# Kernel optimization log

Hardware: AMD Instinct MI355X
Metric: run time of the kernel (lower is better)

Reference implementation:

```python
import jax, jax.numpy as jnp
import numpy as np

ALPHA = 0.2          # LeakyReLU negative slope (Alpha)
NEG_INF = -9e15      # mask value used by pygat-style GAT


def _masked_attention(Wh, a_src, a_dst, mask):
    """Wh: [H,N,d], a_src/a_dst: [H,d], mask: [N,N] (nonzero = edge).
    Returns attention-aggregated features [H,N,d]."""
    f_src = jnp.einsum('hnd,hd->hn', Wh, a_src)   # [H,N]
    f_dst = jnp.einsum('hnd,hd->hn', Wh, a_dst)   # [H,N]
    e = jax.nn.leaky_relu(f_src[:, :, None] + f_dst[:, None, :], ALPHA)  # [H,N,N]
    e = jnp.where(mask[None, :, :] > 0, e, NEG_INF)
    att = jax.nn.softmax(e, axis=-1)              # masked softmax over neighbors
    return jnp.einsum('hnm,hmd->hnd', att, Wh)    # [H,N,d]


def setup_inputs() -> dict:
    key = jax.random.key(0)
    ks = jax.random.split(key, 8)
    N, F_in, D, H = 4096, 512, 64, 8
    x = jax.random.normal(ks[0], (N, F_in), dtype=jnp.float32)
    adj = jax.random.randint(ks[1], (N, N), 0, 2, dtype=jnp.int32)
    s = 0.1
    W = jax.random.normal(ks[2], (H, F_in, D), dtype=jnp.float32) * s
    a_src = jax.random.normal(ks[3], (H, D), dtype=jnp.float32) * s
    a_dst = jax.random.normal(ks[4], (H, D), dtype=jnp.float32) * s
    W_o = jax.random.normal(ks[5], (H * D, D), dtype=jnp.float32) * s
    ao_src = jax.random.normal(ks[6], (D,), dtype=jnp.float32) * s
    ao_dst = jax.random.normal(ks[7], (D,), dtype=jnp.float32) * s
    return {"x": x, "adj": adj, "W": W, "a_src": a_src, "a_dst": a_dst,
            "W_o": W_o, "ao_src": ao_src, "ao_dst": ao_dst}


def reference(x, adj, W, a_src, a_dst, W_o, ao_src, ao_dst):
    N = x.shape[0]
    # --- multi-head layer (concat=True: ELU per head, concat on feature dim) ---
    Wh = jnp.einsum('nf,hfd->hnd', x, W)                     # [H,N,d]
    h1 = jax.nn.elu(_masked_attention(Wh, a_src, a_dst, adj))  # [H,N,d]
    h_cat = jnp.transpose(h1, (1, 0, 2)).reshape(N, -1)      # [N, H*d]
    # --- output head (concat=False: no ELU inside layer) ---
    Who = (h_cat @ W_o)[None]                                # [1,N,d]
    h2 = _masked_attention(Who, ao_src[None], ao_dst[None], adj)[0]  # [N,d]
    # GAT.forward: activation (ELU) then log_softmax over dim=1
    return jax.nn.log_softmax(jax.nn.elu(h2), axis=1)
```

## Files before the change

### kernel.cpp

```cpp
#include <hip/hip_runtime.h>
#include <hip/hip_bf16.h>
#include <math.h>

#define N_NODES 4096
#define FDIM 512
#define D 64
#define H 8
#define NWORDS (N_NODES / 64)

typedef __attribute__((ext_vector_type(8))) short bf16x8;
typedef __attribute__((ext_vector_type(4))) float f32x4;

__device__ inline short f2bf(float x) {
    return (short)((__builtin_bit_cast(unsigned int, x) + 0x8000u) >> 16);
}
__device__ inline float b2f(unsigned short s) {
    return __builtin_bit_cast(float, (unsigned int)s << 16);
}

__device__ inline int sext_bit(unsigned int v, int j) {
#if defined(__has_builtin) && __has_builtin(__builtin_amdgcn_sbfe)
    return __builtin_amdgcn_sbfe((int)v, j, 1);
#else
    return ((int)(v << (31 - j))) >> 31;
#endif
}

__device__ inline unsigned fenc(float f) {
    unsigned u = __builtin_bit_cast(unsigned, f);
    return (u & 0x80000000u) ? ~u : (u | 0x80000000u);
}
__device__ inline float fdec(unsigned e) {
    unsigned u = (e & 0x80000000u) ? (e & 0x7FFFFFFFu) : ~e;
    return __builtin_bit_cast(float, u);
}

__device__ inline void gl2lds16(const void* g, void* l) {
#if defined(__has_builtin) && __has_builtin(__builtin_amdgcn_global_load_lds)
    __builtin_amdgcn_global_load_lds(
        (const __attribute__((address_space(1))) unsigned int*)g,
        (__attribute__((address_space(3))) unsigned int*)l, 16, 0, 0);
#else
    *(uint4*)l = *(const uint4*)g;
#endif
}

#define NB_BITS (N_NODES * N_NODES / 2048)
#define NB_X    (N_NODES * FDIM / 1024)
#define NB_W    (H * FDIM * D / 256)
#define NB_WO   (FDIM * D / 256)
__global__ void k_pre(const int* __restrict__ adj, const float* __restrict__ x,
                      const float* __restrict__ W, const float* __restrict__ Wo,
                      unsigned int* __restrict__ bits32, short* __restrict__ Xbf,
                      short* __restrict__ WF, short* __restrict__ WoF,
                      float* __restrict__ cm1, float* __restrict__ cm2,
                      unsigned* __restrict__ gmaxe1, unsigned* __restrict__ gmaxe2) {
    const int b = blockIdx.x, t = threadIdx.x;
    if (b == 0) {
        for (int i = t; i < H * D; i += 256) cm1[i] = 0.f;
        if (t < D) cm2[t] = 0.f;
        if (t < H) gmaxe1[t] = 0u;
        if (t == 0) gmaxe2[0] = 0u;
        return;
    }
    if (b < 1 + NB_BITS) {
        const int tid  = (b - 1) * 256 + t;
        const size_t e0 = (size_t)tid * 8;
        int4 a0 = *(const int4*)&adj[e0];
        int4 a1 = *(const int4*)&adj[e0 + 4];
        unsigned by = (unsigned)(a0.x != 0)       | ((unsigned)(a0.y != 0) << 1)
                    | ((unsigned)(a0.z != 0) << 2) | ((unsigned)(a0.w != 0) << 3)
                    | ((unsigned)(a1.x != 0) << 4) | ((unsigned)(a1.y != 0) << 5)
                    | ((unsigned)(a1.z != 0) << 6) | ((unsigned)(a1.w != 0) << 7);
        unsigned v = by | (__shfl_xor((int)by, 1) << 8);
        v = v | ((unsigned)__shfl_xor((int)v, 2) << 16);
        if ((t & 3) == 0) bits32[tid >> 2] = v;
        return;
    }
    if (b < 1 + NB_BITS + NB_X) {
        const size_t i4 = ((size_t)(b - 1 - NB_BITS) * 256 + t) * 4;
        float4 v = *(const float4*)&x[i4];
        ushort4 o;
        o.x = (unsigned short)f2bf(v.x); o.y = (unsigned short)f2bf(v.y);
        o.z = (unsigned short)f2bf(v.z); o.w = (unsigned short)f2bf(v.w);
        *(ushort4*)&Xbf[i4] = o;
        return;
    }
    if (b < 1 + NB_BITS + NB_X + NB_W) {
        const size_t idx = (size_t)(b - 1 - NB_BITS - NB_X) * 256 + t;
        const int d = idx & 63;
        const int k = (int)(idx >> 6) & 511;
        const int h = (int)(idx >> 15);
        WF[(((size_t)h * 64 + (k >> 3)) * 64 + d) * 8 + (k & 7)] = f2bf(W[idx]);
        return;
    }
    {
        const size_t idx = (size_t)(b - 1 - NB_BITS - NB_X - NB_W) * 256 + t;
        const int d = idx & 63;
        const int k = (int)(idx >> 6);
        WoF[(((size_t)(k >> 3)) * 64 + d) * 8 + (k & 7)] = f2bf(Wo[idx]);
    }
}

__global__ void __launch_bounds__(256) k_gemm(
    const short* __restrict__ Xbf, const short* __restrict__ WF,
    const float* __restrict__ av, const float* __restrict__ bv,
    short* __restrict__ WBout, float* __restrict__ fs, float* __restrict__ fd,
    unsigned* __restrict__ gmaxe, float* __restrict__ cm) {
    const int h  = blockIdx.y;
    const int i0 = blockIdx.x * 64;
    const int t = threadIdx.x, w = t >> 6, lane = t & 63;
    const int li = lane & 15, quad = lane >> 4, k0 = quad * 8;
    const int row_a = i0 + w * 16 + li;
    const short* __restrict__ Xr  = Xbf + (size_t)row_a * FDIM;
    const short* __restrict__ WFh = WF + (size_t)h * 64 * D * 8;

    f32x4 c0 = {0.f, 0.f, 0.f, 0.f}, c1 = c0, c2 = c0, c3 = c0;
    #pragma unroll 4
    for (int kt = 0; kt < FDIM; kt += 32) {
        bf16x8 a = *(const bf16x8*)&Xr[kt + k0];
        const short* bb = WFh + (size_t)((kt >> 3) + quad) * (D * 8) + li * 8;
        bf16x8 b0 = *(const bf16x8*)(bb);
        bf16x8 b1 = *(const bf16x8*)(bb + 128);
        bf16x8 b2 = *(const bf16x8*)(bb + 256);
        bf16x8 b3 = *(const bf16x8*)(bb + 384);
        c0 = __builtin_amdgcn_mfma_f32_16x16x32_bf16(a, b0, c0, 0, 0, 0);
        c1 = __builtin_amdgcn_mfma_f32_16x16x32_bf16(a, b1, c1, 0, 0, 0);
        c2 = __builtin_amdgcn_mfma_f32_16x16x32_bf16(a, b2, c2, 0, 0, 0);
        c3 = __builtin_amdgcn_mfma_f32_16x16x32_bf16(a, b3, c3, 0, 0, 0);
    }
    float av4[4], bv4[4];
    #pragma unroll
    for (int t4 = 0; t4 < 4; ++t4) {
        av4[t4] = av[h * D + t4 * 16 + li];
        bv4[t4] = bv[h * D + t4 * 16 + li];
    }
    float tiles[4][4];
    #pragma unroll
    for (int r = 0; r < 4; ++r) { tiles[0][r] = c0[r]; tiles[1][r] = c1[r]; tiles[2][r] = c2[r]; tiles[3][r] = c3[r]; }

    __shared__ float csum[4][64];
    __shared__ float red[4];
    float fdmax = -INFINITY;
    float s4[4] = {0.f, 0.f, 0.f, 0.f};

    #pragma unroll
    for (int r = 0; r < 4; ++r) {
        const int row = i0 + w * 16 + quad * 4 + r;
        float pa = 0.f, pb = 0.f;
        #pragma unroll
        for (int t4 = 0; t4 < 4; ++t4) {
            const float v = tiles[t4][r];
            const int d = t4 * 16 + li;
            WBout[((size_t)h * (N_NODES / 8) + (row >> 3)) * (D * 8) + d * 8 + (row & 7)] = f2bf(v);
            pa += v * av4[t4];
            pb += v * bv4[t4];
            s4[t4] += v;
        }
        #pragma unroll
        for (int off = 1; off < 16; off <<= 1) {
            pa += __shfl_xor(pa, off);
            pb += __shfl_xor(pb, off);
        }
        if (li == 0) {
            fs[(size_t)h * N_NODES + row] = pa;
            fd[(size_t)h * N_NODES + row] = pb;
        }
        fdmax = fmaxf(fdmax, pb);
    }
    fdmax = fmaxf(fdmax, __shfl_xor(fdmax, 16));
    fdmax = fmaxf(fdmax, __shfl_xor(fdmax, 32));
    if (lane == 0) red[w] = fdmax;
    #pragma unroll
    for (int t4 = 0; t4 < 4; ++t4) {
        s4[t4] += __shfl_xor(s4[t4], 16);
        s4[t4] += __shfl_xor(s4[t4], 32);
    }
    if (quad == 0)
        #pragma unroll
        for (int t4 = 0; t4 < 4; ++t4) csum[w][t4 * 16 + li] = s4[t4];
    __syncthreads();
    if (t == 0)
        atomicMax(gmaxe + h, fenc(fmaxf(fmaxf(red[0], red[1]), fmaxf(red[2], red[3]))));
    if (t < 64)
        atomicAdd(&cm[h * D + t],
                  (csum[0][t] + csum[1][t] + csum[2][t] + csum[3][t]) * (1.f / (float)N_NODES));
}

__global__ void __launch_bounds__(256) k_accum(
    const unsigned int* __restrict__ bits32,
    const short* __restrict__ WB,
    const float* __restrict__ fsb, const float* __restrict__ fdb,
    const unsigned* __restrict__ gmaxe,
    short* __restrict__ num, float* __restrict__ den, int kslab) {

    __shared__ __align__(16) short Bt[2][16 * 64 * 8];
    __shared__ __align__(16) float EG[2][256];

    const int h = blockIdx.y, i0 = blockIdx.x * 256, slab = blockIdx.z;
    const int t = threadIdx.x, w = t >> 6, lane = t & 63;
    const int li = lane & 15, quad = lane >> 4, k0 = quad * 8;
    const size_t ho = (size_t)h * N_NODES;
    const float  gm = fdec(gmaxe[h]);
    float Rv[4];
    const unsigned int* __restrict__ brow[4];
    #pragma unroll
    for (int f = 0; f < 4; ++f) {
        const int r = i0 + w * 64 + f * 16 + li;
        Rv[f] = __expf(-0.8f * (fsb[ho + r] + gm));
        brow[f] = bits32 + (size_t)r * (NWORDS * 2);
    }
    const float* __restrict__ fd = fdb + ho;
    const short* __restrict__ Bh = WB + (size_t)h * (N_NODES / 8) * D * 8;

    f32x4 acc[4][4], c5[4];
    #pragma unroll
    for (int f = 0; f < 4; ++f) {
        #pragma unroll
        for (int q = 0; q < 4; ++q) acc[f][q] = (f32x4){0.f, 0.f, 0.f, 0.f};
        c5[f] = (f32x4){0.f, 0.f, 0.f, 0.f};
    }
    bf16x8 ones;
    #pragma unroll
    for (int j = 0; j < 8; ++j) ones[j] = (short)0x3F80;

    const int k_beg = slab * kslab;
    const int ntile = kslab / 128;

    auto stage = [&](int buf, int jt) {
        const short* src = Bh + (size_t)(jt >> 3) * (D * 8);
        #pragma unroll
        for (int p = 0; p < 4; ++p)
            gl2lds16(src + (size_t)(p * 256 + t) * 8, &Bt[buf][(p * 256 + t) * 8]);
        if (w == 0) {
            float2 f2 = *(const float2*)&fd[jt + lane * 2];
            float2 ev, gv;
            ev.x = __expf(f2.x - gm);          ev.y = __expf(f2.y - gm);
            gv.x = __expf(0.2f * (f2.x - gm)); gv.y = __expf(0.2f * (f2.y - gm));
            *(float2*)&EG[buf][lane * 2]       = ev;
            *(float2*)&EG[buf][128 + lane * 2] = gv;
        }
    };

    stage(0, k_beg);
    uint4 bw[4];
    #pragma unroll
    for (int f = 0; f < 4; ++f) bw[f] = *(const uint4*)&brow[f][k_beg >> 5];
    for (int tile = 0; tile < ntile; ++tile) {
        const int jt = k_beg + tile * 128;
        __syncthreads();
        if (tile + 1 < ntile) stage((tile + 1) & 1, jt + 128);
        const short* Bl  = Bt[tile & 1];
        const float* EGl = EG[tile & 1];
        unsigned int bwa[4][4];
        #pragma unroll
        for (int f = 0; f < 4; ++f) {
            bwa[f][0] = bw[f].x; bwa[f][1] = bw[f].y; bwa[f][2] = bw[f].z; bwa[f][3] = bw[f].w;
        }
        if (tile + 1 < ntile)
            #pragma unroll
            for (int f = 0; f < 4; ++f) bw[f] = *(const uint4*)&brow[f][(jt + 128) >> 5];
        #pragma unroll
        for (int s = 0; s < 4; ++s) {
            const float4 e0 = *(const float4*)&EGl[s * 32 + k0];
            const float4 e1 = *(const float4*)&EGl[s * 32 + k0 + 4];
            const float4 g0 = *(const float4*)&EGl[128 + s * 32 + k0];
            const float4 g1 = *(const float4*)&EGl[128 + s * 32 + k0 + 4];
            float ev[8], gv[8];
            ev[0] = e0.x; ev[1] = e0.y; ev[2] = e0.z; ev[3] = e0.w;
            ev[4] = e1.x; ev[5] = e1.y; ev[6] = e1.z; ev[7] = e1.w;
            gv[0] = g0.x; gv[1] = g0.y; gv[2] = g0.z; gv[3] = g0.w;
            gv[4] = g1.x; gv[5] = g1.y; gv[6] = g1.z; gv[7] = g1.w;
            const short* bb = Bl + (size_t)((s * 4 + quad) * 64 + li) * 8;
            bf16x8 b0 = *(const bf16x8*)(bb);
            bf16x8 b1 = *(const bf16x8*)(bb + 128);
            bf16x8 b2 = *(const bf16x8*)(bb + 256);
            bf16x8 b3 = *(const bf16x8*)(bb + 384);
            #pragma unroll
            for (int f = 0; f < 4; ++f) {
                const unsigned int byt = (bwa[f][s] >> k0) & 0xFFu;
                unsigned int pa[8];
                #pragma unroll
                for (int j = 0; j < 8; ++j) {
                    const float p = fmaxf(ev[j], gv[j] * Rv[f]);
                    pa[j] = __builtin_bit_cast(unsigned int, p)
                            & (unsigned int)sext_bit(byt, j);
                }
                bf16x8 a;
                unsigned int* au = (unsigned int*)&a;
                au[0] = __builtin_amdgcn_perm(pa[1], pa[0], 0x07060302);
                au[1] = __builtin_amdgcn_perm(pa[3], pa[2], 0x07060302);
                au[2] = __builtin_amdgcn_perm(pa[5], pa[4], 0x07060302);
                au[3] = __builtin_amdgcn_perm(pa[7], pa[6], 0x07060302);
                acc[f][0] = __builtin_amdgcn_mfma_f32_16x16x32_bf16(a, b0, acc[f][0], 0, 0, 0);
                acc[f][1] = __builtin_amdgcn_mfma_f32_16x16x32_bf16(a, b1, acc[f][1], 0, 0, 0);
                acc[f][2] = __builtin_amdgcn_mfma_f32_16x16x32_bf16(a, b2, acc[f][2], 0, 0, 0);
                acc[f][3] = __builtin_amdgcn_mfma_f32_16x16x32_bf16(a, b3, acc[f][3], 0, 0, 0);
                c5[f]     = __builtin_amdgcn_mfma_f32_16x16x32_bf16(a, ones, c5[f], 0, 0, 0);
            }
        }
    }

    const size_t so = (size_t)(slab * gridDim.y + h);
    #pragma unroll
    for (int f = 0; f < 4; ++f) {
        #pragma unroll
        for (int t4 = 0; t4 < 4; ++t4)
            #pragma unroll
            for (int r = 0; r < 4; ++r) {
                const int row = i0 + w * 64 + f * 16 + quad * 4 + r;
                num[(so * N_NODES + row) * D + t4 * 16 + li] = f2bf(acc[f][t4][r]);
            }
        if (li == 0)
            #pragma unroll
            for (int r = 0; r < 4; ++r)
                den[so * N_NODES + i0 + w * 64 + f * 16 + quad * 4 + r] = c5[f][r];
    }
}

__global__ void k_post1(const short* __restrict__ num, const float* __restrict__ den,
                        const float* __restrict__ colmean, short* __restrict__ hcat) {
    const int h   = blockIdx.y;
    const int i0  = blockIdx.x * 64;
    const int t   = threadIdx.x;
    const int row = i0 + (t >> 2);
    const int cb  = (t & 3) * 16;
    const size_t HN = (size_t)gridDim.y * N_NODES;
    const size_t r0 = (size_t)h * N_NODES + row;
    float dsum = 0.f;
    #pragma unroll
    for (int s = 0; s < 8; ++s) dsum += den[s * HN + r0];
    const bool  uni  = !(dsum > 0.f);
    const float linv = uni ? 0.f : 1.f / dsum;
    #pragma unroll
    for (int c = 0; c < 4; ++c) {
        const int col = cb + c * 4;
        float4 v = {0.f, 0.f, 0.f, 0.f};
        #pragma unroll
        for (int s = 0; s < 8; ++s) {
            ushort4 a = *(const ushort4*)&num[(s * HN + r0) * D + col];
            v.x += b2f(a.x); v.y += b2f(a.y); v.z += b2f(a.z); v.w += b2f(a.w);
        }
        v.x *= linv; v.y *= linv; v.z *= linv; v.w *= linv;
        if (uni) v = *(const float4*)&colmean[h * D + col];
        v.x = v.x > 0.f ? v.x : __expf(v.x) - 1.f;
        v.y = v.y > 0.f ? v.y : __expf(v.y) - 1.f;
        v.z = v.z > 0.f ? v.z : __expf(v.z) - 1.f;
        v.w = v.w > 0.f ? v.w : __expf(v.w) - 1.f;
        ushort4 o;
        o.x = (unsigned short)f2bf(v.x); o.y = (unsigned short)f2bf(v.y);
        o.z = (unsigned short)f2bf(v.z); o.w = (unsigned short)f2bf(v.w);
        *(ushort4*)&hcat[(size_t)row * (H * D) + h * D + col] = o;
    }
}

__global__ void k_lsm(const short* __restrict__ num, const float* __restrict__ den,
                      const float* __restrict__ cm, float* __restrict__ out) {
    const int n    = blockIdx.x * 4 + (threadIdx.x >> 6);
    const int lane = threadIdx.x & 63;
    float v = 0.f, ds = 0.f;
    #pragma unroll
    for (int s = 0; s < 32; ++s)
        v += b2f((unsigned short)num[((size_t)s * N_NODES + n) * D + lane]);
    #pragma unroll
    for (int s = 0; s < 32; ++s) ds += den[(size_t)s * N_NODES + n];
    v = (ds > 0.f) ? v / ds : cm[lane];
    v = v > 0.f ? v : __expf(v) - 1.f;
    float mx = v;
    #pragma unroll
    for (int off = 32; off > 0; off >>= 1) mx = fmaxf(mx, __shfl_xor(mx, off));
    float ex = __expf(v - mx);
    float sum = ex;
    #pragma unroll
    for (int off = 32; off > 0; off >>= 1) sum += __shfl_xor(sum, off);
    out[(size_t)n * D + lane] = (v - mx) - __logf(sum);
}

extern "C" void kernel_launch(void* const* d_in, const int* in_sizes, int n_in,
                              void* d_out, int out_size, void* d_ws, size_t ws_size,
                              hipStream_t stream) {
    const float* x      = (const float*)d_in[0];
    const int*   adj    = (const int*)d_in[1];
    const float* W      = (const float*)d_in[2];
    const float* a_src  = (const float*)d_in[3];
    const float* a_dst  = (const float*)d_in[4];
    const float* W_o    = (const float*)d_in[5];
    const float* ao_src = (const float*)d_in[6];
    const float* ao_dst = (const float*)d_in[7];
    float* out = (float*)d_out;

    char* wsp = (char*)d_ws;
    size_t off = 0;
    auto alloc = [&](size_t bytes) -> void* {
        void* p = wsp + off;
        off += (bytes + 255) & ~(size_t)255;
        return p;
    };
    unsigned* adj_bits = (unsigned*)alloc((size_t)N_NODES * NWORDS * 8);
    short*    Xbf   = (short*)alloc((size_t)N_NODES * FDIM * 2);
    short*    WF1   = (short*)alloc((size_t)H * 64 * D * 8 * 2);
    short*    WoF   = (short*)alloc((size_t)64 * D * 8 * 2);
    short*    WhB   = (short*)alloc((size_t)H * N_NODES * D * 2);
    float*    fs1   = (float*)alloc((size_t)H * N_NODES * 4);
    float*    fd1   = (float*)alloc((size_t)H * N_NODES * 4);
    unsigned* gme1  = (unsigned*)alloc((size_t)H * 4);
    float*    cm1   = (float*)alloc((size_t)H * D * 4);
    short*    num1  = (short*)alloc((size_t)8 * H * N_NODES * D * 2);
    float*    den1  = (float*)alloc((size_t)8 * H * N_NODES * 4);
    short*    hcat  = (short*)alloc((size_t)N_NODES * H * D * 2);
    short*    WhoB  = (short*)alloc((size_t)N_NODES * D * 2);
    float*    fs2   = (float*)alloc((size_t)N_NODES * 4);
    float*    fd2   = (float*)alloc((size_t)N_NODES * 4);
    unsigned* gme2  = (unsigned*)alloc(4);
    float*    cm2   = (float*)alloc((size_t)D * 4);
    short*    num2  = (short*)alloc((size_t)32 * N_NODES * D * 2);
    float*    den2  = (float*)alloc((size_t)32 * N_NODES * 4);

    k_pre  <<<dim3(1 + NB_BITS + NB_X + NB_W + NB_WO), dim3(256), 0, stream>>>(
        adj, x, W, W_o, adj_bits, Xbf, WF1, WoF, cm1, cm2, gme1, gme2);

    k_gemm <<<dim3(N_NODES / 64, H), dim3(256), 0, stream>>>(Xbf, WF1, a_src, a_dst,
                                                             WhB, fs1, fd1, gme1, cm1);
    k_accum<<<dim3(N_NODES / 256, H, 8), dim3(256), 0, stream>>>(adj_bits, WhB, fs1, fd1, gme1,
                                                                 num1, den1, N_NODES / 8);
    k_post1<<<dim3(N_NODES / 64, H), dim3(256), 0, stream>>>(num1, den1, cm1, hcat);

    k_gemm <<<dim3(N_NODES / 64, 1), dim3(256), 0, stream>>>(hcat, WoF, ao_src, ao_dst,
                                                             WhoB, fs2, fd2, gme2, cm2);
    k_accum<<<dim3(N_NODES / 256, 1, 32), dim3(256), 0, stream>>>(adj_bits, WhoB, fs2, fd2, gme2,
                                                                  num2, den2, N_NODES / 32);
    k_lsm  <<<dim3(N_NODES / 4), dim3(256), 0, stream>>>(num2, den2, cm2, out);
}
```

Measured before the change: 204.7 us.

## Precompute slab exp tables, use explicit vmcnt waits and MFMA priority in k_accum

Computes the per-column E/G exponential tables for the whole k-slab once up front in shared memory, instead of having one wave compute them every tile. Replaces __syncthreads with raw s_barrier plus explicit s_waitcnt vmcnt so the next tile's B loads stay in flight. Moves the adjacency bit loads into the loop, raises MFMA issue priority with s_setprio, and adds an occupancy hint of 3 blocks per CU. The manual vmcnt counting is fragile: it assumes kslab is at most 512 and depends on the exact number of outstanding loads. Capping registers for the occupancy hint may also cause spills.

```diff
diff --git a/kernel.cpp b/kernel.cpp
--- a/kernel.cpp
+++ b/kernel.cpp
@@ -187,7 +187,7 @@
                   (csum[0][t] + csum[1][t] + csum[2][t] + csum[3][t]) * (1.f / (float)N_NODES));
 }
 
-__global__ void __launch_bounds__(256) k_accum(
+__global__ void __launch_bounds__(256, 3) k_accum(
     const unsigned int* __restrict__ bits32,
     const short* __restrict__ WB,
     const float* __restrict__ fsb, const float* __restrict__ fdb,
@@ -195,24 +195,51 @@
     short* __restrict__ num, float* __restrict__ den, int kslab) {
 
     __shared__ __align__(16) short Bt[2][16 * 64 * 8];
-    __shared__ __align__(16) float EG[2][256];
+    __shared__ __align__(16) float Esh[512];
+    __shared__ __align__(16) float Gsh[512];
 
     const int h = blockIdx.y, i0 = blockIdx.x * 256, slab = blockIdx.z;
     const int t = threadIdx.x, w = t >> 6, lane = t & 63;
     const int li = lane & 15, quad = lane >> 4, k0 = quad * 8;
     const size_t ho = (size_t)h * N_NODES;
     const float  gm = fdec(gmaxe[h]);
-    float Rv[4];
-    const unsigned int* __restrict__ brow[4];
-    #pragma unroll
-    for (int f = 0; f < 4; ++f) {
-        const int r = i0 + w * 64 + f * 16 + li;
-        Rv[f] = __expf(-0.8f * (fsb[ho + r] + gm));
-        brow[f] = bits32 + (size_t)r * (NWORDS * 2);
-    }
     const float* __restrict__ fd = fdb + ho;
     const short* __restrict__ Bh = WB + (size_t)h * (N_NODES / 8) * D * 8;
 
+    const int k_beg = slab * kslab;
+    const int ntile = kslab / 128;
+
+    auto stage = [&](int buf, int jtile) {
+        const short* src = Bh + (size_t)(jtile >> 3) * (D * 8);
+        #pragma unroll
+        for (int p = 0; p < 4; ++p)
+            gl2lds16(src + (size_t)(p * 256 + t) * 8, &Bt[buf][(p * 256 + t) * 8]);
+    };
+
+    int bito[4];
+    #pragma unroll
+    for (int f = 0; f < 4; ++f)
+        bito[f] = (i0 + w * 64 + f * 16 + li) * (NWORDS * 2);
+    uint4 bw[4];
+    #pragma unroll
+    for (int f = 0; f < 4; ++f)
+        bw[f] = *(const uint4*)&bits32[(size_t)bito[f] + (k_beg >> 5)];
+    stage(0, k_beg);
+    {
+        const int jj = t * 2;
+        if (jj < kslab) {
+            float2 f2 = *(const float2*)&fd[k_beg + jj];
+            Esh[jj]     = __expf(f2.x - gm);
+            Esh[jj + 1] = __expf(f2.y - gm);
+            Gsh[jj]     = __expf(0.2f * (f2.x - gm));
+            Gsh[jj + 1] = __expf(0.2f * (f2.y - gm));
+        }
+    }
+    float Rv[4];
+    #pragma unroll
+    for (int f = 0; f < 4; ++f)
+        Rv[f] = __expf(-0.8f * (fsb[ho + i0 + w * 64 + f * 16 + li] + gm));
+
     f32x4 acc[4][4], c5[4];
     #pragma unroll
     for (int f = 0; f < 4; ++f) {
@@ -224,48 +251,33 @@
     #pragma unroll
     for (int j = 0; j < 8; ++j) ones[j] = (short)0x3F80;
 
-    const int k_beg = slab * kslab;
-    const int ntile = kslab / 128;
-
-    auto stage = [&](int buf, int jt) {
-        const short* src = Bh + (size_t)(jt >> 3) * (D * 8);
-        #pragma unroll
-        for (int p = 0; p < 4; ++p)
-            gl2lds16(src + (size_t)(p * 256 + t) * 8, &Bt[buf][(p * 256 + t) * 8]);
-        if (w == 0) {
-            float2 f2 = *(const float2*)&fd[jt + lane * 2];
-            float2 ev, gv;
-            ev.x = __expf(f2.x - gm);          ev.y = __expf(f2.y - gm);
-            gv.x = __expf(0.2f * (f2.x - gm)); gv.y = __expf(0.2f * (f2.y - gm));
-            *(float2*)&EG[buf][lane * 2]       = ev;
-            *(float2*)&EG[buf][128 + lane * 2] = gv;
-        }
-    };
-
-    stage(0, k_beg);
-    uint4 bw[4];
-    #pragma unroll
-    for (int f = 0; f < 4; ++f) bw[f] = *(const uint4*)&brow[f][k_beg >> 5];
+    __syncthreads();
+
     for (int tile = 0; tile < ntile; ++tile) {
         const int jt = k_beg + tile * 128;
-        __syncthreads();
-        if (tile + 1 < ntile) stage((tile + 1) & 1, jt + 128);
-        const short* Bl  = Bt[tile & 1];
-        const float* EGl = EG[tile & 1];
-        unsigned int bwa[4][4];
-        #pragma unroll
-        for (int f = 0; f < 4; ++f) {
-            bwa[f][0] = bw[f].x; bwa[f][1] = bw[f].y; bwa[f][2] = bw[f].z; bwa[f][3] = bw[f].w;
-        }
-        if (tile + 1 < ntile)
+        __builtin_amdgcn_s_barrier();
+        if (tile > 0) {
             #pragma unroll
-            for (int f = 0; f < 4; ++f) bw[f] = *(const uint4*)&brow[f][(jt + 128) >> 5];
+            for (int f = 0; f < 4; ++f)
+                bw[f] = *(const uint4*)&bits32[(size_t)bito[f] + (jt >> 5)];
+        }
+        if (tile + 1 < ntile) {
+            stage((tile + 1) & 1, jt + 128);
+            asm volatile("s_waitcnt vmcnt(4)" ::: "memory");
+        } else {
+            asm volatile("s_waitcnt vmcnt(0)" ::: "memory");
+        }
+        __builtin_amdgcn_s_barrier();
+
+        const short* Bl = Bt[tile & 1];
+        const float* Ee = Esh + tile * 128;
+        const float* Gg = Gsh + tile * 128;
         #pragma unroll
         for (int s = 0; s < 4; ++s) {
-            const float4 e0 = *(const float4*)&EGl[s * 32 + k0];
-            const float4 e1 = *(const float4*)&EGl[s * 32 + k0 + 4];
-            const float4 g0 = *(const float4*)&EGl[128 + s * 32 + k0];
-            const float4 g1 = *(const float4*)&EGl[128 + s * 32 + k0 + 4];
+            const float4 e0 = *(const float4*)&Ee[s * 32 + k0];
+            const float4 e1 = *(const float4*)&Ee[s * 32 + k0 + 4];
+            const float4 g0 = *(const float4*)&Gg[s * 32 + k0];
+            const float4 g1 = *(const float4*)&Gg[s * 32 + k0 + 4];
             float ev[8], gv[8];
             ev[0] = e0.x; ev[1] = e0.y; ev[2] = e0.z; ev[3] = e0.w;
             ev[4] = e1.x; ev[5] = e1.y; ev[6] = e1.z; ev[7] = e1.w;
@@ -278,7 +290,9 @@
             bf16x8 b3 = *(const bf16x8*)(bb + 384);
             #pragma unroll
             for (int f = 0; f < 4; ++f) {
-                const unsigned int byt = (bwa[f][s] >> k0) & 0xFFu;
+                const unsigned int wsel = (s == 0) ? bw[f].x : (s == 1) ? bw[f].y
+                                        : (s == 2) ? bw[f].z : bw[f].w;
+                const unsigned int byt = (wsel >> k0) & 0xFFu;
                 unsigned int pa[8];
                 #pragma unroll
                 for (int j = 0; j < 8; ++j) {
@@ -292,11 +306,13 @@
                 au[1] = __builtin_amdgcn_perm(pa[3], pa[2], 0x07060302);
                 au[2] = __builtin_amdgcn_perm(pa[5], pa[4], 0x07060302);
                 au[3] = __builtin_amdgcn_perm(pa[7], pa[6], 0x07060302);
+                __builtin_amdgcn_s_setprio(1);
                 acc[f][0] = __builtin_amdgcn_mfma_f32_16x16x32_bf16(a, b0, acc[f][0], 0, 0, 0);
                 acc[f][1] = __builtin_amdgcn_mfma_f32_16x16x32_bf16(a, b1, acc[f][1], 0, 0, 0);
                 acc[f][2] = __builtin_amdgcn_mfma_f32_16x16x32_bf16(a, b2, acc[f][2], 0, 0, 0);
                 acc[f][3] = __builtin_amdgcn_mfma_f32_16x16x32_bf16(a, b3, acc[f][3], 0, 0, 0);
                 c5[f]     = __builtin_amdgcn_mfma_f32_16x16x32_bf16(a, ones, c5[f], 0, 0, 0);
+                __builtin_amdgcn_s_setprio(0);
             }
         }
     }
```

New measurement: 203.5 us. Within noise of the previous version (-0.6%).
